# Kernel optimization log

Measured on AMD Instinct MI355X. Metric: run time of the kernel, lower is better.

## Reference

```python
import jax, jax.numpy as jnp
import numpy as np

H = 16       # num_attention_heads
DH = 64      # attention_head_size
D = H * DH   # hidden_size = 1024
SCALE = DH ** -0.5


def setup_inputs() -> dict:
    key = jax.random.key(0)
    ks = jax.random.split(key, 9)
    s = 0.02
    return {
        "hidden_states": jax.random.normal(ks[0], (2, 2048, D), jnp.float32),
        "Wq": jax.random.normal(ks[1], (D, D), jnp.float32) * s,
        "bq": jax.random.normal(ks[2], (D,), jnp.float32) * s,
        "Wk": jax.random.normal(ks[3], (D, D), jnp.float32) * s,
        "bk": jax.random.normal(ks[4], (D,), jnp.float32) * s,
        "Wv": jax.random.normal(ks[5], (D, D), jnp.float32) * s,
        "bv": jax.random.normal(ks[6], (D,), jnp.float32) * s,
        "Wo": jax.random.normal(ks[7], (D, D), jnp.float32) * s,
        "bo": jax.random.normal(ks[8], (D,), jnp.float32) * s,
    }


def reference(hidden_states, Wq, bq, Wk, bk, Wv, bv, Wo, bo):
    B, S, _ = hidden_states.shape
    # project and split into heads: [B, H, S, DH]
    def heads(x):
        return x.reshape(B, S, H, DH).transpose(0, 2, 1, 3)
    q = heads(hidden_states @ Wq + bq)
    k = heads(hidden_states @ Wk + bk)
    v = heads(hidden_states @ Wv + bv)
    # eager attention: full [B,H,S,S] scores, softmax in fp32
    scores = jnp.einsum("bhqd,bhkd->bhqk", q, k) * SCALE
    probs = jax.nn.softmax(scores.astype(jnp.float32), axis=-1).astype(q.dtype)
    ctx = jnp.einsum("bhqk,bhkd->bqhd", probs, v).reshape(B, S, D)
    # output projection (dropout inactive at eval)
    return ctx @ Wo + bo
```

## Files before the change

### kernel.cpp

```cpp
#include <hip/hip_runtime.h>

typedef __bf16 bf16;
typedef __bf16 bf16x8 __attribute__((ext_vector_type(8)));
typedef __bf16 bf16x4 __attribute__((ext_vector_type(4)));
typedef __bf16 bf16x2 __attribute__((ext_vector_type(2)));
typedef float  f32x4  __attribute__((ext_vector_type(4)));
typedef unsigned u32x2 __attribute__((ext_vector_type(2)));
typedef unsigned u32x4 __attribute__((ext_vector_type(4)));

#define DEV __device__ __forceinline__

DEV int detect_f32(const void* x) {
  const unsigned short* u = (const unsigned short*)x;
  int lane = threadIdx.x & 63;
  int e = (u[lane * 8] >> 7) & 0xFF;
  unsigned long long b = __ballot(e >= 118 && e <= 134);
  return __popcll(b) < 32;
}

DEV void gl2lds16(const bf16* g, bf16* l) {
  __builtin_amdgcn_global_load_lds(
      (const __attribute__((address_space(1))) void*)g,
      (__attribute__((address_space(3))) void*)l, 16, 0, 0);
}

DEV unsigned pack_bf16(float a, float b) {
  bf16x2 t;
  t[0] = (bf16)a;
  t[1] = (bf16)b;
  return __builtin_bit_cast(unsigned, t);
}

__global__ __launch_bounds__(256) void prep(
    const void* __restrict__ X, const void* __restrict__ bq,
    const void* __restrict__ bk, const void* __restrict__ bv,
    const void* __restrict__ bo, const void* __restrict__ Wq,
    const void* __restrict__ Wk, const void* __restrict__ Wv,
    const void* __restrict__ Wo, bf16* __restrict__ Xb,
    bf16* __restrict__ bqkv, bf16* __restrict__ bob,
    bf16* __restrict__ Wtqkv, bf16* __restrict__ Wto) {
  __shared__ __align__(16) bf16 T[64 * 80];
  int f32 = detect_f32(X);
  int blk = blockIdx.x, tid = threadIdx.x;
  if (blk < 2048) {
    long base = (long)blk * 2048 + tid * 8;
    bf16x8 o;
    if (f32) {
      const float* s = (const float*)X + base;
#pragma unroll
      for (int i = 0; i < 8; ++i) o[i] = (bf16)s[i];
    } else {
      o = *(const bf16x8*)((const bf16*)X + base);
    }
    *(bf16x8*)&Xb[base] = o;
  } else if (blk < 2052) {
    const void* src = (blk == 2048) ? bq : (blk == 2049) ? bk : (blk == 2050) ? bv : bo;
    bf16* dst = (blk == 2051) ? bob : bqkv + (blk - 2048) * 1024;
    int base = tid * 4;
    if (f32) {
      const float* s = (const float*)src;
#pragma unroll
      for (int i = 0; i < 4; ++i) dst[base + i] = (bf16)s[base + i];
    } else {
      const bf16* s = (const bf16*)src;
#pragma unroll
      for (int i = 0; i < 4; ++i) dst[base + i] = s[base + i];
    }
  } else {
    int id = blk - 2052;
    int z = id >> 8, r = id & 255;
    int k0 = (r & 15) * 64, n0 = (r >> 4) * 64;
    const void* src = (z == 0) ? Wq : (z == 1) ? Wk : (z == 2) ? Wv : Wo;
    bf16* dst = (z < 3) ? (Wtqkv + (long)z * 1048576) : Wto;
#pragma unroll
    for (int c = 0; c < 2; ++c) {
      int lin = tid + c * 256;
      int row = lin >> 3, col8 = (lin & 7) * 8;
      long gidx = (long)(k0 + row) * 1024 + n0 + col8;
      bf16x8 v;
      if (f32) {
        const float* s = (const float*)src + gidx;
#pragma unroll
        for (int i = 0; i < 8; ++i) v[i] = (bf16)s[i];
      } else {
        v = *(const bf16x8*)((const bf16*)src + gidx);
      }
      *(bf16x8*)&T[row * 80 + col8] = v;
    }
    __syncthreads();
#pragma unroll
    for (int c = 0; c < 2; ++c) {
      int lin = tid + c * 256;
      int row = lin >> 3, col8 = (lin & 7) * 8;
      bf16x8 v;
#pragma unroll
      for (int i = 0; i < 8; ++i) v[i] = T[(col8 + i) * 80 + row];
      *(bf16x8*)&dst[(long)(n0 + row) * 1024 + k0 + col8] = v;
    }
  }
}

template <int TM, int TN, int MODE>
__global__ __launch_bounds__(256, 3) void gemm_bt(
    const bf16* __restrict__ A, const bf16* __restrict__ Bt, int M, int N,
    int K, void* __restrict__ Cout, const bf16* __restrict__ bias,
    const void* __restrict__ detect_src, bf16* __restrict__ Qo,
    bf16* __restrict__ Ko, bf16* __restrict__ Vo) {
  constexpr int NWN = TN / 64;
  constexpr int NWM = 4 / NWN;
  constexpr int MT = TM / (NWM * 16);
  __shared__ __align__(16) bf16 GS[TM * 64 + TN * 64];
  bf16* As = GS;
  bf16* Bs = GS + TM * 64;
  int tid = threadIdx.x, lane = tid & 63, wave = tid >> 6;
  int quad = lane >> 4, l16 = lane & 15;
  int m0 = blockIdx.x * TM, n0 = blockIdx.y * TN;
  int wm = (wave / NWN) * (TM / NWM), wn = (wave % NWN) * 64;
  f32x4 zero = {0.f, 0.f, 0.f, 0.f};
  f32x4 acc[MT][4];
#pragma unroll
  for (int i = 0; i < MT; ++i)
#pragma unroll
    for (int j = 0; j < 4; ++j) acc[i][j] = zero;

  for (int k0 = 0; k0 < K; k0 += 64) {
#pragma unroll
    for (int i = 0; i < TM / 32; ++i) {
      int u = (i * 4 + wave) * 64 + lane;
      int r = u >> 3, g = (u & 7) ^ (r & 7);
      gl2lds16(A + (long)(m0 + r) * K + k0 + g * 8, As + (i * 4 + wave) * 512);
    }
#pragma unroll
    for (int i = 0; i < TN / 32; ++i) {
      int u = (i * 4 + wave) * 64 + lane;
      int r = u >> 3, g = (u & 7) ^ (r & 7);
      gl2lds16(Bt + (long)(n0 + r) * K + k0 + g * 8, Bs + (i * 4 + wave) * 512);
    }
    __syncthreads();
#pragma unroll
    for (int kc = 0; kc < 2; ++kc) {
      bf16x8 bv_[4];
#pragma unroll
      for (int nt = 0; nt < 4; ++nt) {
        int row = wn + nt * 16 + l16;
        bv_[nt] = *(const bf16x8*)&Bs[row * 64 + (((kc * 4 + quad) ^ (l16 & 7))) * 8];
      }
#pragma unroll
      for (int mt = 0; mt < MT; ++mt) {
        int row = wm + mt * 16 + l16;
        bf16x8 af = *(const bf16x8*)&As[row * 64 + (((kc * 4 + quad) ^ (l16 & 7))) * 8];
#pragma unroll
        for (int nt = 0; nt < 4; ++nt)
          acc[mt][nt] = __builtin_amdgcn_mfma_f32_16x16x32_bf16(bv_[nt], af,
                                                                acc[mt][nt], 0, 0, 0);
      }
    }
    __syncthreads();
  }

  if (MODE == 0) {
    int f32o = detect_f32(detect_src);
#pragma unroll
    for (int nt = 0; nt < 4; ++nt) {
      int n = n0 + wn + nt * 16 + quad * 4;
      bf16x4 bb = *(const bf16x4*)&bias[n];
#pragma unroll
      for (int mt = 0; mt < MT; ++mt) {
        int m = m0 + wm + mt * 16 + l16;
        if (f32o) {
          f32x4 v;
#pragma unroll
          for (int r = 0; r < 4; ++r) v[r] = acc[mt][nt][r] + (float)bb[r];
          *(f32x4*)((float*)Cout + (long)m * N + n) = v;
        } else {
          bf16x4 v;
#pragma unroll
          for (int r = 0; r < 4; ++r) v[r] = (bf16)(acc[mt][nt][r] + (float)bb[r]);
          *(bf16x4*)((bf16*)Cout + (long)m * N + n) = v;
        }
      }
    }
  } else {
    int t = n0 >> 10;
    if (t < 2) {
      float qsc = (t == 0) ? 0.1803368801f : 1.0f;
      bf16* op = (t == 0) ? Qo : Ko;
#pragma unroll
      for (int nt = 0; nt < 4; ++nt) {
        int n = n0 + wn + nt * 16 + quad * 4;
        bf16x4 bb = *(const bf16x4*)&bias[n];
        int nl = n & 1023, h = nl >> 6, dh = nl & 63;
#pragma unroll
        for (int mt = 0; mt < MT; ++mt) {
          int m = m0 + wm + mt * 16 + l16;
          int b = m >> 11, s = m & 2047;
          bf16x4 v;
#pragma unroll
          for (int r = 0; r < 4; ++r)
            v[r] = (bf16)((acc[mt][nt][r] + (float)bb[r]) * qsc);
          *(bf16x4*)&op[((long)(b * 16 + h) * 2048 + s) * 64 + dh] = v;
        }
      }
    } else {
      bf16* T = GS;
#pragma unroll
      for (int nt = 0; nt < 4; ++nt) {
        int n = wn + nt * 16 + quad * 4;
        bf16x4 bb = *(const bf16x4*)&bias[n0 + n];
#pragma unroll
        for (int mt = 0; mt < MT; ++mt) {
          int m = wm + mt * 16 + l16;
#pragma unroll
          for (int r = 0; r < 4; ++r)
            T[(n + r) * 128 + m] = (bf16)(acc[mt][nt][r] + (float)bb[r]);
        }
      }
      __syncthreads();
      int b = m0 >> 11, s0 = m0 & 2047;
      int h0 = (n0 & 1023) >> 6;
#pragma unroll
      for (int c = 0; c < 8; ++c) {
        int u = c * 256 + tid;
        int row = u >> 4, col = (u & 15) * 8;
        bf16x8 v = *(const bf16x8*)&T[row * 128 + col];
        long base =
            ((long)(b * 16 + h0 + (row >> 6)) * 64 + (row & 63)) * 2048 + s0;
        *(bf16x8*)&Vo[base + col] = v;
      }
    }
  }
}

__global__ __launch_bounds__(512, 4) void attn(const bf16* __restrict__ Qg,
                                               const bf16* __restrict__ Kg,
                                               const bf16* __restrict__ Vtg,
                                               bf16* __restrict__ ctx) {
  __shared__ __align__(16) bf16 SMEM[32768];
  bf16* Ksh = SMEM;
  bf16* Vsh = SMEM + 16384;
  float* MG = (float*)SMEM;

  int tid = threadIdx.x, lane = tid & 63, w = tid >> 6;
  int grp = w >> 2, wq = w & 3;
  int quad = lane >> 4, l16 = lane & 15;
  int lin = blockIdx.x | (blockIdx.y << 4);
  int swz = ((lin & 7) << 6) | (lin >> 3);
  int bh = swz >> 4, q0 = (swz & 15) << 7;
  const bf16* Qh = Qg + (long)bh * 131072;
  const bf16* Kh = Kg + (long)bh * 131072;
  const bf16* Vh = Vtg + (long)bh * 131072;
  int qbase = q0 + wq * 32;

  bf16x8 qf[2][2];
#pragma unroll
  for (int nt = 0; nt < 2; ++nt)
#pragma unroll
    for (int kc = 0; kc < 2; ++kc)
      qf[nt][kc] = *(const bf16x8*)&Qh[(long)(qbase + nt * 16 + l16) * 64 +
                                       kc * 32 + quad * 8];

  int e0 = l16 * 64 + (quad ^ (l16 & 7)) * 8;
  int e1 = l16 * 64 + ((4 + quad) ^ (l16 & 7)) * 8;

  int mS = tid >> 3, gS = (tid & 7) ^ (mS & 7);
  int kvpS = (mS & 32) + ((mS & 12) << 1) + ((mS & 16) >> 2) + (mS & 3);
  int koff = kvpS * 64 + gS * 8;
  int voff = mS * 2048 + gS * 8;
  int ldsoff = tid * 8;

  auto stage1 = [&](int t) {
    int buf = t & 3;
    gl2lds16(Kh + (long)t * 4096 + koff, Ksh + buf * 4096 + ldsoff);
    gl2lds16(Vh + t * 64 + voff, Vsh + buf * 4096 + ldsoff);
  };

  bf16x8 onesv;
#pragma unroll
  for (int i = 0; i < 8; ++i) onesv[i] = (bf16)1.0f;

  f32x4 zero = {0.f, 0.f, 0.f, 0.f};
  f32x4 O[2][4];
  f32x4 Ol[2] = {zero, zero};
#pragma unroll
  for (int i = 0; i < 2; ++i)
#pragma unroll
    for (int j = 0; j < 4; ++j) O[i][j] = zero;

  auto compute = [&](const bf16* Kb, const bf16* Vb) {
    u32x2 pk[4][2];
#pragma unroll
    for (int mt = 0; mt < 4; ++mt) {
      bf16x8 kf0 = *(const bf16x8*)&Kb[e0 + mt * 1024];
      bf16x8 kf1 = *(const bf16x8*)&Kb[e1 + mt * 1024];
#pragma unroll
      for (int nt = 0; nt < 2; ++nt) {
        f32x4 s_ = zero;
        __builtin_amdgcn_s_setprio(1);
        s_ = __builtin_amdgcn_mfma_f32_16x16x32_bf16(kf0, qf[nt][0], s_, 0, 0, 0);
        s_ = __builtin_amdgcn_mfma_f32_16x16x32_bf16(kf1, qf[nt][1], s_, 0, 0, 0);
        __builtin_amdgcn_s_setprio(0);
        f32x4 p;
        p[0] = __builtin_amdgcn_exp2f(s_[0]);
        p[1] = __builtin_amdgcn_exp2f(s_[1]);
        p[2] = __builtin_amdgcn_exp2f(s_[2]);
        p[3] = __builtin_amdgcn_exp2f(s_[3]);
        pk[mt][nt][0] = pack_bf16(p[0], p[1]);
        pk[mt][nt][1] = pack_bf16(p[2], p[3]);
      }
    }
#pragma unroll
    for (int c = 0; c < 2; ++c) {
      bf16x8 pb[2];
#pragma unroll
      for (int nt = 0; nt < 2; ++nt) {
        u32x4 tt;
        tt[0] = pk[2 * c][nt][0];
        tt[1] = pk[2 * c][nt][1];
        tt[2] = pk[2 * c + 1][nt][0];
        tt[3] = pk[2 * c + 1][nt][1];
        pb[nt] = __builtin_bit_cast(bf16x8, tt);
      }
      int ec = c ? e1 : e0;
      __builtin_amdgcn_s_setprio(1);
#pragma unroll
      for (int dt = 0; dt < 4; ++dt) {
        bf16x8 vf = *(const bf16x8*)&Vb[ec + dt * 1024];
#pragma unroll
        for (int nt = 0; nt < 2; ++nt)
          O[nt][dt] = __builtin_amdgcn_mfma_f32_16x16x32_bf16(vf, pb[nt],
                                                              O[nt][dt], 0, 0, 0);
      }
#pragma unroll
      for (int nt = 0; nt < 2; ++nt)
        Ol[nt] = __builtin_amdgcn_mfma_f32_16x16x32_bf16(onesv, pb[nt],
                                                         Ol[nt], 0, 0, 0);
      __builtin_amdgcn_s_setprio(0);
    }
  };

  stage1(0);
  stage1(1);
  for (int it = 0; it < 16; ++it) {
    __syncthreads();
    int ta = 2 * it + 2;
    if (ta < 32) {
      stage1(ta);
      stage1(ta + 1);
    }
    int t = 2 * it + grp;
    compute(Ksh + (t & 3) * 4096, Vsh + (t & 3) * 4096);
  }

  float lsum[2] = {Ol[0][0], Ol[1][0]};

  __syncthreads();
  float* Mp = MG + wq * 2176;
  if (grp == 1) {
#pragma unroll
    for (int nt = 0; nt < 2; ++nt) {
#pragma unroll
      for (int dt = 0; dt < 4; ++dt)
        *(f32x4*)&Mp[((nt * 4 + dt) * 64 + lane) * 4] = O[nt][dt];
      Mp[2048 + nt * 64 + lane] = lsum[nt];
    }
  }
  __syncthreads();
  if (grp == 0) {
#pragma unroll
    for (int nt = 0; nt < 2; ++nt) {
#pragma unroll
      for (int dt = 0; dt < 4; ++dt) {
        f32x4 o2 = *(const f32x4*)&Mp[((nt * 4 + dt) * 64 + lane) * 4];
#pragma unroll
        for (int r = 0; r < 4; ++r) O[nt][dt][r] += o2[r];
      }
      lsum[nt] += Mp[2048 + nt * 64 + lane];
    }
    float rv[2];
#pragma unroll
    for (int nt = 0; nt < 2; ++nt) rv[nt] = __builtin_amdgcn_rcpf(lsum[nt]);
    int b = bh >> 4, h = bh & 15;
#pragma unroll
    for (int nt = 0; nt < 2; ++nt) {
      int s = qbase + nt * 16 + l16;
#pragma unroll
      for (int dt = 0; dt < 4; ++dt) {
        bf16x4 v;
#pragma unroll
        for (int r = 0; r < 4; ++r) v[r] = (bf16)(O[nt][dt][r] * rv[nt]);
        *(bf16x4*)&ctx[((long)(b * 2048 + s)) * 1024 + h * 64 + dt * 16 +
                       quad * 4] = v;
      }
    }
  }
}

extern "C" void kernel_launch(void* const* d_in, const int* in_sizes, int n_in,
                              void* d_out, int out_size, void* d_ws,
                              size_t ws_size, hipStream_t stream) {
  const void* X  = d_in[0];
  const void* Wq = d_in[1]; const void* bq = d_in[2];
  const void* Wk = d_in[3]; const void* bk = d_in[4];
  const void* Wv = d_in[5]; const void* bv = d_in[6];
  const void* Wo = d_in[7]; const void* bo = d_in[8];

  char* ws = (char*)d_ws;
  bf16* Xb    = (bf16*)(ws);
  bf16* Wtqkv = (bf16*)(ws + 8388608);
  bf16* Wto   = (bf16*)(ws + 14680064);
  bf16* bqkv  = (bf16*)(ws + 16777216);
  bf16* bob   = (bf16*)(ws + 16783360);
  bf16* Qw    = (bf16*)(ws + 16785408);
  bf16* Kw    = (bf16*)(ws + 25174016);
  bf16* Cx    = (bf16*)(ws + 33562624);
  bf16* Vt    = (bf16*)(ws + 41951232);

  prep<<<dim3(3076), 256, 0, stream>>>(X, bq, bk, bv, bo, Wq, Wk, Wv, Wo, Xb,
                                       bqkv, bob, Wtqkv, Wto);
  gemm_bt<128, 128, 1><<<dim3(32, 24), 256, 0, stream>>>(
      Xb, Wtqkv, 4096, 3072, 1024, nullptr, bqkv, nullptr, Qw, Kw, Vt);
  attn<<<dim3(16, 32), 512, 0, stream>>>(Qw, Kw, Vt, Cx);
  gemm_bt<128, 64, 0><<<dim3(32, 16), 256, 0, stream>>>(
      Cx, Wto, 4096, 1024, 1024, d_out, bob, X, nullptr, nullptr, nullptr);
}
```

Baseline: 181.1 us.

## Swizzle GEMM blocks across XCDs and restructure attention inner loop and epilogue

The GEMM kernel remaps its linear block index in groups of eight, so that neighbouring output tiles on the same XCD share A/B rows and columns in L2. The attention compute loop now runs the QK^T and exp step for each half of the key tile right before its PV MFMAs, which shortens the life of the probability registers. The final merge of the two wave groups is split so that each group reduces and writes one of the two query subtiles, instead of one group doing all of it. Risks: the swizzle assumes the block count is divisible by eight, and indexing the register arrays with a runtime value could push them to scratch memory.

After: 190.3 us. 1.05x slower.

```diff
diff --git a/kernel.cpp b/kernel.cpp
--- a/kernel.cpp
+++ b/kernel.cpp
@@ -114,7 +114,11 @@
   bf16* Bs = GS + TM * 64;
   int tid = threadIdx.x, lane = tid & 63, wave = tid >> 6;
   int quad = lane >> 4, l16 = lane & 15;
-  int m0 = blockIdx.x * TM, n0 = blockIdx.y * TN;
+  int lin = blockIdx.x + blockIdx.y * gridDim.x;
+  int cpx = (gridDim.x * gridDim.y) >> 3;
+  int swz = (lin & 7) * cpx + (lin >> 3);
+  int bx = swz % gridDim.x, by = swz / gridDim.x;
+  int m0 = bx * TM, n0 = by * TN;
   int wm = (wave / NWN) * (TM / NWM), wn = (wave % NWN) * 64;
   f32x4 zero = {0.f, 0.f, 0.f, 0.f};
   f32x4 acc[MT][4];
@@ -287,53 +291,42 @@
     for (int j = 0; j < 4; ++j) O[i][j] = zero;
 
   auto compute = [&](const bf16* Kb, const bf16* Vb) {
-    u32x2 pk[4][2];
-#pragma unroll
-    for (int mt = 0; mt < 4; ++mt) {
-      bf16x8 kf0 = *(const bf16x8*)&Kb[e0 + mt * 1024];
-      bf16x8 kf1 = *(const bf16x8*)&Kb[e1 + mt * 1024];
-#pragma unroll
-      for (int nt = 0; nt < 2; ++nt) {
-        f32x4 s_ = zero;
-        __builtin_amdgcn_s_setprio(1);
-        s_ = __builtin_amdgcn_mfma_f32_16x16x32_bf16(kf0, qf[nt][0], s_, 0, 0, 0);
-        s_ = __builtin_amdgcn_mfma_f32_16x16x32_bf16(kf1, qf[nt][1], s_, 0, 0, 0);
-        __builtin_amdgcn_s_setprio(0);
-        f32x4 p;
-        p[0] = __builtin_amdgcn_exp2f(s_[0]);
-        p[1] = __builtin_amdgcn_exp2f(s_[1]);
-        p[2] = __builtin_amdgcn_exp2f(s_[2]);
-        p[3] = __builtin_amdgcn_exp2f(s_[3]);
-        pk[mt][nt][0] = pack_bf16(p[0], p[1]);
-        pk[mt][nt][1] = pack_bf16(p[2], p[3]);
-      }
-    }
 #pragma unroll
     for (int c = 0; c < 2; ++c) {
-      bf16x8 pb[2];
-#pragma unroll
-      for (int nt = 0; nt < 2; ++nt) {
-        u32x4 tt;
-        tt[0] = pk[2 * c][nt][0];
-        tt[1] = pk[2 * c][nt][1];
-        tt[2] = pk[2 * c + 1][nt][0];
-        tt[3] = pk[2 * c + 1][nt][1];
-        pb[nt] = __builtin_bit_cast(bf16x8, tt);
-      }
+      u32x4 pw[2];
+#pragma unroll
+      for (int m2 = 0; m2 < 2; ++m2) {
+        int mt = c * 2 + m2;
+        bf16x8 kf0 = *(const bf16x8*)&Kb[e0 + mt * 1024];
+        bf16x8 kf1 = *(const bf16x8*)&Kb[e1 + mt * 1024];
+#pragma unroll
+        for (int nt = 0; nt < 2; ++nt) {
+          f32x4 s_ = zero;
+          __builtin_amdgcn_s_setprio(1);
+          s_ = __builtin_amdgcn_mfma_f32_16x16x32_bf16(kf0, qf[nt][0], s_, 0, 0, 0);
+          s_ = __builtin_amdgcn_mfma_f32_16x16x32_bf16(kf1, qf[nt][1], s_, 0, 0, 0);
+          __builtin_amdgcn_s_setprio(0);
+          f32x4 p;
+          p[0] = __builtin_amdgcn_exp2f(s_[0]);
+          p[1] = __builtin_amdgcn_exp2f(s_[1]);
+          p[2] = __builtin_amdgcn_exp2f(s_[2]);
+          p[3] = __builtin_amdgcn_exp2f(s_[3]);
+          pw[nt][m2 * 2]     = pack_bf16(p[0], p[1]);
+          pw[nt][m2 * 2 + 1] = pack_bf16(p[2], p[3]);
+        }
+      }
+      bf16x8 pb0 = __builtin_bit_cast(bf16x8, pw[0]);
+      bf16x8 pb1 = __builtin_bit_cast(bf16x8, pw[1]);
       int ec = c ? e1 : e0;
       __builtin_amdgcn_s_setprio(1);
 #pragma unroll
       for (int dt = 0; dt < 4; ++dt) {
         bf16x8 vf = *(const bf16x8*)&Vb[ec + dt * 1024];
-#pragma unroll
-        for (int nt = 0; nt < 2; ++nt)
-          O[nt][dt] = __builtin_amdgcn_mfma_f32_16x16x32_bf16(vf, pb[nt],
-                                                              O[nt][dt], 0, 0, 0);
-      }
-#pragma unroll
-      for (int nt = 0; nt < 2; ++nt)
-        Ol[nt] = __builtin_amdgcn_mfma_f32_16x16x32_bf16(onesv, pb[nt],
-                                                         Ol[nt], 0, 0, 0);
+        O[0][dt] = __builtin_amdgcn_mfma_f32_16x16x32_bf16(vf, pb0, O[0][dt], 0, 0, 0);
+        O[1][dt] = __builtin_amdgcn_mfma_f32_16x16x32_bf16(vf, pb1, O[1][dt], 0, 0, 0);
+      }
+      Ol[0] = __builtin_amdgcn_mfma_f32_16x16x32_bf16(onesv, pb0, Ol[0], 0, 0, 0);
+      Ol[1] = __builtin_amdgcn_mfma_f32_16x16x32_bf16(onesv, pb1, Ol[1], 0, 0, 0);
       __builtin_amdgcn_s_setprio(0);
     }
   };
@@ -355,43 +348,29 @@
 
   __syncthreads();
   float* Mp = MG + wq * 2176;
-  if (grp == 1) {
-#pragma unroll
-    for (int nt = 0; nt < 2; ++nt) {
-#pragma unroll
-      for (int dt = 0; dt < 4; ++dt)
-        *(f32x4*)&Mp[((nt * 4 + dt) * 64 + lane) * 4] = O[nt][dt];
-      Mp[2048 + nt * 64 + lane] = lsum[nt];
-    }
-  }
+  int nte = 1 - grp, ntf = grp;
+#pragma unroll
+  for (int dt = 0; dt < 4; ++dt)
+    *(f32x4*)&Mp[((nte * 4 + dt) * 64 + lane) * 4] = O[nte][dt];
+  Mp[2048 + nte * 64 + lane] = lsum[nte];
   __syncthreads();
-  if (grp == 0) {
-#pragma unroll
-    for (int nt = 0; nt < 2; ++nt) {
-#pragma unroll
-      for (int dt = 0; dt < 4; ++dt) {
-        f32x4 o2 = *(const f32x4*)&Mp[((nt * 4 + dt) * 64 + lane) * 4];
-#pragma unroll
-        for (int r = 0; r < 4; ++r) O[nt][dt][r] += o2[r];
-      }
-      lsum[nt] += Mp[2048 + nt * 64 + lane];
-    }
-    float rv[2];
-#pragma unroll
-    for (int nt = 0; nt < 2; ++nt) rv[nt] = __builtin_amdgcn_rcpf(lsum[nt]);
-    int b = bh >> 4, h = bh & 15;
-#pragma unroll
-    for (int nt = 0; nt < 2; ++nt) {
-      int s = qbase + nt * 16 + l16;
-#pragma unroll
-      for (int dt = 0; dt < 4; ++dt) {
-        bf16x4 v;
-#pragma unroll
-        for (int r = 0; r < 4; ++r) v[r] = (bf16)(O[nt][dt][r] * rv[nt]);
-        *(bf16x4*)&ctx[((long)(b * 2048 + s)) * 1024 + h * 64 + dt * 16 +
-                       quad * 4] = v;
-      }
-    }
+#pragma unroll
+  for (int dt = 0; dt < 4; ++dt) {
+    f32x4 o2 = *(const f32x4*)&Mp[((ntf * 4 + dt) * 64 + lane) * 4];
+#pragma unroll
+    for (int r = 0; r < 4; ++r) O[ntf][dt][r] += o2[r];
+  }
+  float ls = lsum[ntf] + Mp[2048 + ntf * 64 + lane];
+  float rv = __builtin_amdgcn_rcpf(ls);
+  int b = bh >> 4, h = bh & 15;
+  int s = qbase + ntf * 16 + l16;
+#pragma unroll
+  for (int dt = 0; dt < 4; ++dt) {
+    bf16x4 v;
+#pragma unroll
+    for (int r = 0; r < 4; ++r) v[r] = (bf16)(O[ntf][dt][r] * rv);
+    *(bf16x4*)&ctx[((long)(b * 2048 + s)) * 1024 + h * 64 + dt * 16 +
+                   quad * 4] = v;
   }
 }
 
```
